# Optimization experiments

Hardware: AMD Instinct MI355X
Metric: run time of the kernel (lower is better)

Reference implementation:

```python
import jax, jax.numpy as jnp
import numpy as np

KERNEL = 10   # kernel_size (asserted == 10 in the original)
HEADS = 4
BN_SCALE = 1.0 / np.sqrt(1.0 + 1e-5)  # eval-mode BatchNorm1d (running mean 0, var 1, affine 1/0)


def get_dct_matrix(N):
    k = np.arange(N)[:, None].astype(np.float64)
    i = np.arange(N)[None, :].astype(np.float64)
    w = np.full((N, 1), np.sqrt(2.0 / N))
    w[0, 0] = np.sqrt(1.0 / N)
    dct_m = w * np.cos(np.pi * (i + 0.5) * k / N)
    idct_m = np.linalg.inv(dct_m)
    return dct_m.astype(np.float32), idct_m.astype(np.float32)


def conv1d(x, w):  # x [B,C,L], w [O,I,K], valid, no bias
    return jax.lax.conv_general_dilated(x, w, (1,), 'VALID',
                                        dimension_numbers=('NCH', 'OIH', 'NCH'))


def conv_stack(x, w1, w2):  # Conv1d(k=6) -> ReLU -> Conv1d(k=5) -> ReLU
    return jax.nn.relu(conv1d(jax.nn.relu(conv1d(x, w1)), w2))


# vmap over the 4 heads' weights -> [H,B,D,L]
heads_conv = jax.vmap(conv_stack, in_axes=(None, 0, 0))


def _forward(src, cq1, cq2, ck1, ck2, lw, lb, giw, gia, gib, gbw, gba, gbb,
             gow, goa, gob, dct_n, output_n, input_n):
    bs, in_feat = src.shape[0], src.shape[2]
    src = src[:, :input_n]                                   # [B,50,48]
    src_key = jnp.swapaxes(src, 1, 2)[:, :, :input_n - output_n]  # [B,48,25]
    src_query = jnp.swapaxes(src, 1, 2)[:, :, -KERNEL:]           # [B,48,10]

    dct_np, idct_np = get_dct_matrix(KERNEL + output_n)
    dct_m = jnp.asarray(dct_np)
    idct_m = jnp.asarray(idct_np)

    vn = input_n - KERNEL - output_n + 1  # 16 overlapping value windows
    vl = KERNEL + output_n                # window length 35
    idx = np.arange(vl)[None, :] + np.arange(vn)[:, None]    # [16,35]
    windows = src[:, idx]                                    # [B,16,35,48]
    # DCT per window then flatten per-joint coeffs: [B,16,48*dct_n]
    val = jnp.einsum('dv,bnvf->bndf', dct_m[:dct_n], windows)
    src_value = jnp.swapaxes(val, 2, 3).reshape(bs, vn, -1)  # [B,16,480]

    key_h = heads_conv(src_key / 1000.0, ck1, ck2)           # [H,B,512,16]
    query_h = heads_conv(src_query / 1000.0, cq1, cq2)       # [H,B,512,1]

    # sum-normalized (non-softmax) attention
    score = jnp.einsum('hbdq,hbdk->hbqk', query_h, key_h) + 1e-15  # [H,B,1,16]
    att_w = score / jnp.sum(score, axis=3, keepdims=True)
    dct_att = jnp.einsum('hbk,bkf->hbf', att_w[:, :, 0], src_value)  # [H,B,480]
    dct_att = dct_att.reshape(HEADS, bs, in_feat, dct_n)
    att_cat = jnp.transpose(dct_att, (1, 0, 2, 3)).reshape(bs, HEADS * in_feat, dct_n)
    # Linear over the concatenated head/joint axis: [B,48,dct_n]
    att_lin = jnp.einsum('bmd,nm->bnd', att_cat, lw) + lb[None, :, None]

    # last kernel_size frames + last frame repeated output_n times
    gather_idx = np.concatenate([np.arange(input_n - KERNEL, input_n),
                                 np.full(output_n, input_n - 1)])
    input_gcn = src[:, gather_idx]                           # [B,35,48]
    dct_in = jnp.einsum('dv,bvf->bfd', dct_m[:dct_n], input_gcn)  # [B,48,10]
    dct_in = jnp.concatenate([dct_in, att_lin], axis=-1)     # [B,48,20]

    # GCN (Mao et al. style): learnable adjacency [48,48], eval-mode BN, tanh
    def gc(h, a, w, b):
        return jnp.einsum('nm,bmf->bnf', a, h @ w) + b

    y = jnp.tanh(gc(dct_in, gia, giw, gib) * BN_SCALE)       # [B,48,512]
    for s in range(gbw.shape[0]):
        r = y
        for j in range(2):
            y = jnp.tanh(gc(y, gba[s, j], gbw[s, j], gbb[s, j]) * BN_SCALE)
        y = y + r
    dct_out = gc(y, goa, gow, gob) + dct_in                  # [B,48,20]

    out_gcn = jnp.einsum('vd,bnd->bvn', idct_m[:, :dct_n], dct_out[:, :, :dct_n])  # [B,35,48]
    return out_gcn[:, :, None, :]                            # [B,35,itera=1,48]


def setup_inputs() -> dict:
    key = jax.random.key(0)
    ks = jax.random.split(key, 16)
    bs, in_feat, d_model, dct_n = 256, 48, 512, 10
    s = 0.05
    return {
        'src': jax.random.normal(ks[0], (bs, 50, in_feat), jnp.float32) * 1000.0,
        'convQ_w1': jax.random.normal(ks[1], (HEADS, d_model, in_feat, 6), jnp.float32) * s,
        'convQ_w2': jax.random.normal(ks[2], (HEADS, d_model, d_model, 5), jnp.float32) * s,
        'convK_w1': jax.random.normal(ks[3], (HEADS, d_model, in_feat, 6), jnp.float32) * s,
        'convK_w2': jax.random.normal(ks[4], (HEADS, d_model, d_model, 5), jnp.float32) * s,
        'linear_w': jax.random.normal(ks[5], (in_feat, HEADS * in_feat), jnp.float32) * s,
        'linear_b': jax.random.normal(ks[6], (in_feat,), jnp.float32) * s,
        'gc_in_w': jax.random.normal(ks[7], (2 * dct_n, d_model), jnp.float32) * s,
        'gc_in_att': jax.random.normal(ks[8], (in_feat, in_feat), jnp.float32) * s,
        'gc_in_b': jax.random.normal(ks[9], (d_model,), jnp.float32) * s,
        'gcb_w': jax.random.normal(ks[10], (2, 2, d_model, d_model), jnp.float32) * s,
        'gcb_att': jax.random.normal(ks[11], (2, 2, in_feat, in_feat), jnp.float32) * s,
        'gcb_b': jax.random.normal(ks[12], (2, 2, d_model), jnp.float32) * s,
        'gc_out_w': jax.random.normal(ks[13], (d_model, 2 * dct_n), jnp.float32) * s,
        'gc_out_att': jax.random.normal(ks[14], (in_feat, in_feat), jnp.float32) * s,
        'gc_out_b': jax.random.normal(ks[15], (2 * dct_n,), jnp.float32) * s,
        'dct_n': 10, 'output_n': 25, 'input_n': 50, 'itera': 1,
    }


def reference(src, convQ_w1, convQ_w2, convK_w1, convK_w2, linear_w, linear_b,
              gc_in_w, gc_in_att, gc_in_b, gcb_w, gcb_att, gcb_b,
              gc_out_w, gc_out_att, gc_out_b, dct_n, output_n, input_n, itera):
    # itera=1 path only (itera>1 in the original references undefined attrs)
    return _forward(src, convQ_w1, convQ_w2, convK_w1, convK_w2, linear_w, linear_b,
                    gc_in_w, gc_in_att, gc_in_b, gcb_w, gcb_att, gcb_b,
                    gc_out_w, gc_out_att, gc_out_b, dct_n, output_n, input_n)
```

## Files before the change

### kernel.cpp

```cpp
#include <hip/hip_runtime.h>
#include <math.h>

static constexpr float BN_SCALE_F = 0.9999950000374997f;

typedef __bf16 bf16;
typedef bf16 bf16x8 __attribute__((ext_vector_type(8)));
typedef bf16 bf16x4 __attribute__((ext_vector_type(4)));
typedef float floatx4 __attribute__((ext_vector_type(4)));

#define GLOBAL_AS __attribute__((address_space(1)))
#define LDS_AS __attribute__((address_space(3)))

__device__ __forceinline__ float tanh_fast(float x) {
    const float e = __expf(2.f * x);
    return 1.f - 2.f / (e + 1.f);
}

__global__ __launch_bounds__(256) void k_prep(
    const float* __restrict__ src, const float* __restrict__ cq1,
    const float* __restrict__ ck1, const float* __restrict__ cq2,
    const float* __restrict__ ck2, const float* __restrict__ gbw,
    const float* __restrict__ giw, const float* __restrict__ gow,
    const float* __restrict__ gba, float* __restrict__ dct10,
    bf16* __restrict__ srcbf, bf16* __restrict__ w1tq, bf16* __restrict__ w1tk,
    bf16* __restrict__ w2tq, bf16* __restrict__ w2tk, bf16* __restrict__ gbwF,
    bf16* __restrict__ giwF, bf16* __restrict__ gowT, bf16* __restrict__ gbaP) {
    __shared__ __align__(16) float lds[10240];
    int bb = blockIdx.x;
    const int t = threadIdx.x;
    if (bb < 2) {
        int id = bb * 256 + t;
        if (id < 350) {
            int k = id / 35, i = id % 35;
            double w = (k == 0) ? sqrt(1.0 / 35.0) : sqrt(2.0 / 35.0);
            dct10[id] = (float)(w * cos(3.14159265358979323846 * (i + 0.5) * k / 35.0));
        }
        return;
    }
    bb -= 2;
    if (bb < 601) {
        const int id4 = (bb * 256 + t) * 4;
        if (id4 + 3 < 614400) {
            const float4 v = *(const float4*)(src + id4);
            bf16x4 ov;
            ov[0] = (bf16)v.x; ov[1] = (bf16)v.y;
            ov[2] = (bf16)v.z; ov[3] = (bf16)v.w;
            *(bf16x4*)(srcbf + id4) = ov;
        } else if (id4 < 614656) {
#pragma unroll
            for (int j = 0; j < 4; ++j) {
                const int id = id4 + j;
                if (id < 614656) srcbf[id] = (bf16)(id < 614400 ? src[id] : 0.f);
            }
        }
        return;
    }
    bb -= 601;
    if (bb < 1280) {
        const bool isQ = bb < 640;
        const float* w = isQ ? cq1 : ck1;
        bf16* wt = isQ ? w1tq : w1tk;
        const int lb = isQ ? bb : bb - 640;
        const int id4 = (lb * 256 + t) * 4;
        const int ho = id4 / 320, c0 = id4 % 320;
        bf16x4 ov;
#pragma unroll
        for (int j = 0; j < 4; ++j) {
            const int c = c0 + j;
            const float v =
                (c < 288) ? w[(long)ho * 288 + (c % 48) * 6 + (c / 48)] * 1e-3f : 0.f;
            ov[j] = (bf16)v;
        }
        *(bf16x4*)(wt + id4) = ov;
        return;
    }
    bb -= 1280;
    if (bb < 1024) {
        const bool isQ = bb < 512;
        const int rb = isQ ? bb : bb - 512;
        const float* wrow = (isQ ? cq2 : ck2) + (long)rb * 4 * 2560;
        bf16* orow = (isQ ? w2tq : w2tk) + (long)rb * 4 * 2560;
        float4* l4 = (float4*)lds;
        const float4* w4 = (const float4*)wrow;
#pragma unroll
        for (int i = 0; i < 10; ++i) l4[t + i * 256] = w4[t + i * 256];
        __syncthreads();
        for (int c = t * 4; c < 10240; c += 1024) {
            const int r = c / 2560, cc = c % 2560;
            const int k = cc >> 9, ii = cc & 511;
            bf16x4 ov;
#pragma unroll
            for (int j = 0; j < 4; ++j)
                ov[j] = (bf16)lds[r * 2560 + (ii + j) * 5 + k];
            *(bf16x4*)(orow + c) = ov;
        }
        return;
    }
    bb -= 1024;
    if (bb < 256) {
        const int l = bb >> 6, tile = bb & 63;
        const int tr = tile >> 3, tc = tile & 7;
        const float* in = gbw + (long)l * 262144;
        bf16* o = gbwF + (long)l * 262144;
#pragma unroll
        for (int r = 0; r < 16; ++r) {
            const int kl = (t >> 6) * 16 + r, ml = t & 63;
            lds[kl * 65 + ml] = in[(long)(tr * 64 + kl) * 512 + tc * 64 + ml];
        }
        __syncthreads();
        for (int j = t; j < 4096; j += 256) {
            const int q = j >> 9, r4 = j & 511;
            const int gl = q >> 2, sl = (q >> 1) & 1, jt = q & 1;
            const int lane = r4 >> 3, e = r4 & 7;
            const int fr = lane & 15, fq = lane >> 4;
            const int kk = sl * 32 + fq * 8 + e;
            const int ff = gl * 32 + jt * 16 + fr;
            o[(long)(tc * 2 + gl) * 16384 + (long)(tr * 2 + sl) * 1024 + jt * 512 + r4] =
                (bf16)lds[kk * 65 + ff];
        }
        return;
    }
    bb -= 256;
    if (bb < 32) {
        const int id4 = (bb * 256 + t) * 4;
        const int g = id4 >> 11, r2 = id4 & 2047;
        const int s = r2 >> 10, r3 = r2 & 1023;
        const int jt = r3 >> 9, r4 = r3 & 511;
        const int lane = r4 >> 3, e0 = r4 & 7;
        const int fr = lane & 15, fq = lane >> 4;
        const int f = g * 32 + jt * 16 + fr;
        bf16x4 ov;
#pragma unroll
        for (int j = 0; j < 4; ++j) {
            const int k = s * 32 + fq * 8 + e0 + j;
            ov[j] = (bf16)(k < 20 ? giw[k * 512 + f] : 0.f);
        }
        *(bf16x4*)(giwF + id4) = ov;
        return;
    }
    bb -= 32;
    if (bb < 16) {
        const int id4 = (bb * 256 + t) * 4;
        const int d = id4 >> 9, k0 = id4 & 511;
        bf16x4 ov;
#pragma unroll
        for (int j = 0; j < 4; ++j)
            ov[j] = (bf16)(d < 20 ? gow[(k0 + j) * 20 + d] : 0.f);
        *(bf16x4*)(gowT + id4) = ov;
        return;
    }
    bb -= 16;
    {
        const int id4 = (bb * 256 + t) * 4;
        const int l = id4 / 3072, r = id4 % 3072;
        const int n = r >> 6, m0 = r & 63;
        bf16x4 ov;
#pragma unroll
        for (int j = 0; j < 4; ++j) {
            const int m = m0 + j;
            ov[j] = (bf16)(m < 48 ? gba[l * 2304 + n * 48 + m] : 0.f);
        }
        *(bf16x4*)(gbaP + id4) = ov;
    }
}

__global__ __launch_bounds__(256) void k_conv1(
    const bf16* __restrict__ w1tk, const bf16* __restrict__ w1tq,
    const bf16* __restrict__ srcbf, bf16* __restrict__ r1k,
    bf16* __restrict__ r1q) {
    int bx, by, bz;
    const bf16* A;
    bf16* C;
    int NT, toff;
    long cStr;
    {
        const int i = blockIdx.x;
        if (i < 1280) {
            bz = i / 320;
            const int r = i % 320;
            bx = r % 40;
            by = r / 40;
            A = w1tk; C = r1k; NT = 20; toff = 0; cStr = 2621440L;
        } else {
            const int j = i - 1280;
            bz = j / 80;
            const int r = j % 80;
            bx = r % 10;
            by = r / 10;
            A = w1tq; C = r1q; NT = 5; toff = 40; cStr = 655360L;
        }
    }
    __shared__ bf16 As[64 * 64];
    __shared__ bf16 Bs[128 * 64];
    const int tid = threadIdx.x;
    const int wave = tid >> 6;
    const int lane = tid & 63;
    const int wm = (wave & 1) * 32;
    const int wn = (wave >> 1) * 64;
    const int m0 = by * 64;
    const int n0 = bx * 128;
    A += (long)bz * (512L * 320);

    const int srow = lane >> 3;
    const int gch = (lane & 7) ^ srow;
    const bf16* aptr[2];
    const bf16* bptr[4];
#pragma unroll
    for (int i = 0; i < 2; ++i) {
        const int ar = wave * 16 + i * 8 + srow;
        aptr[i] = A + (long)(m0 + ar) * 320 + gch * 8;
    }
#pragma unroll
    for (int i = 0; i < 4; ++i) {
        const int ar = wave * 32 + i * 8 + srow;
        const int n = n0 + ar;
        const long bbase = (long)(n / NT) * 2400 + (long)((n % NT) + toff) * 48;
        bptr[i] = srcbf + bbase + gch * 8;
    }

    floatx4 acc[4][2];
#pragma unroll
    for (int j = 0; j < 4; ++j)
#pragma unroll
        for (int i = 0; i < 2; ++i) acc[j][i] = (floatx4){0.f, 0.f, 0.f, 0.f};

    const int fr = lane & 15;
    const int fq = lane >> 4;
    const int fx = lane & 7;

    for (int k0 = 0; k0 < 320; k0 += 64) {
#pragma unroll
        for (int i = 0; i < 2; ++i)
            __builtin_amdgcn_global_load_lds(
                (const GLOBAL_AS void*)(aptr[i] + k0),
                (LDS_AS void*)(As + (wave * 16 + i * 8) * 64), 16, 0, 0);
#pragma unroll
        for (int i = 0; i < 4; ++i)
            __builtin_amdgcn_global_load_lds(
                (const GLOBAL_AS void*)(bptr[i] + k0),
                (LDS_AS void*)(Bs + (wave * 32 + i * 8) * 64), 16, 0, 0);
        __syncthreads();
#pragma unroll
        for (int kk = 0; kk < 2; ++kk) {
            bf16x8 af[2], bfr[4];
#pragma unroll
            for (int im = 0; im < 2; ++im)
                af[im] = *(const bf16x8*)(As + (wm + im * 16 + fr) * 64 +
                                          ((((kk << 2) + fq) ^ fx) << 3));
#pragma unroll
            for (int in = 0; in < 4; ++in)
                bfr[in] = *(const bf16x8*)(Bs + (wn + in * 16 + fr) * 64 +
                                           ((((kk << 2) + fq) ^ fx) << 3));
#pragma unroll
            for (int in = 0; in < 4; ++in)
#pragma unroll
                for (int im = 0; im < 2; ++im)
                    acc[in][im] = __builtin_amdgcn_mfma_f32_16x16x32_bf16(
                        af[im], bfr[in], acc[in][im], 0, 0, 0);
        }
        __syncthreads();
    }
#pragma unroll
    for (int in = 0; in < 4; ++in) {
        const long n = n0 + wn + in * 16 + fr;
#pragma unroll
        for (int im = 0; im < 2; ++im) {
            floatx4 v = acc[in][im];
            const long m = m0 + wm + im * 16 + (fq << 2);
            v.x = fmaxf(v.x, 0.f);
            v.y = fmaxf(v.y, 0.f);
            v.z = fmaxf(v.z, 0.f);
            v.w = fmaxf(v.w, 0.f);
            bf16* Cp = C + (long)bz * cStr + n * 512 + m;
            bf16x4 ov;
            ov[0] = (bf16)v.x;
            ov[1] = (bf16)v.y;
            ov[2] = (bf16)v.z;
            ov[3] = (bf16)v.w;
            *(bf16x4*)Cp = ov;
        }
    }
}

__global__ __launch_bounds__(256) void k_conv2(
    const bf16* __restrict__ w2tk, const bf16* __restrict__ r1k,
    bf16* __restrict__ keyh, const bf16* __restrict__ w2tq,
    const bf16* __restrict__ r1q, bf16* __restrict__ qh) {
    const int K = 2560;
    int bx, by, bz;
    const bf16 *A, *B;
    bf16* C;
    bool kMode;
    long aStr, bStr, cStr;
    {
        const int i = blockIdx.x;
        if (i < 1024) {
            const int slot = i & 7;
            bz = slot >> 1;
            const int half = slot & 1;
            const int j = i >> 3;
            bx = half * 16 + (j & 15);
            by = j >> 4;
            A = w2tk; B = r1k; C = keyh; kMode = true;
            aStr = 512L * 2560; bStr = 2621440L; cStr = 2097152L;
        } else {
            const int j = i - 1024;
            bz = j >> 4;
            const int r = j & 15;
            bx = r & 1;
            by = r >> 1;
            A = w2tq; B = r1q; C = qh; kMode = false;
            aStr = 512L * 2560; bStr = 655360L; cStr = 131072L;
        }
    }
    __shared__ bf16 As[64 * 64];
    __shared__ bf16 Bs[160 * 64];
    const int tid = threadIdx.x;
    const int wave = tid >> 6;
    const int lane = tid & 63;
    const int wm = (wave & 1) * 32;
    const int wn = (wave >> 1) * 64;
    const int m0 = by * 64;
    const int n0 = bx * 128;
    A += (long)bz * aStr;
    B += (long)bz * bStr;

    const int srow = lane >> 3;
    const int gch = (lane & 7) ^ srow;
    const bf16* aptr[2];
#pragma unroll
    for (int i = 0; i < 2; ++i) {
        const int ar = wave * 16 + i * 8 + srow;
        aptr[i] = A + (long)(m0 + ar) * K + gch * 8;
    }

    floatx4 acc[4][2];
#pragma unroll
    for (int j = 0; j < 4; ++j)
#pragma unroll
        for (int i = 0; i < 2; ++i) acc[j][i] = (floatx4){0.f, 0.f, 0.f, 0.f};

    const int fr = lane & 15;
    const int fq = lane >> 4;
    const int fx = lane & 7;

    if (kMode) {
        const bf16* bptrK[5];
        int ldsBK[5];
#pragma unroll
        for (int j = 0; j < 5; ++j) {
            const int rloc = wave * 40 + j * 8 + srow;
            const int brel = rloc / 20, pos = rloc % 20;
            bptrK[j] = B + ((long)((bx * 8 + brel) * 20 + pos)) * 512 +
                       ((lane & 7) ^ (pos & 7)) * 8;
            ldsBK[j] = rloc * 64 + (lane & 7) * 8;
        }
        const int bq = wn >> 4;
        for (int c0i = 0; c0i < 8; ++c0i) {
            const int c0 = c0i * 64;
#pragma unroll
            for (int w = 0; w < 5; ++w) {
                const int k0 = w * 512 + c0;
#pragma unroll
                for (int i = 0; i < 2; ++i)
                    __builtin_amdgcn_global_load_lds(
                        (const GLOBAL_AS void*)(aptr[i] + k0),
                        (LDS_AS void*)(As + (wave * 16 + i * 8) * 64), 16, 0, 0);
                if (w == 0) {
#pragma unroll
                    for (int j = 0; j < 5; ++j)
                        __builtin_amdgcn_global_load_lds(
                            (const GLOBAL_AS void*)(bptrK[j] + c0),
                            (LDS_AS void*)(Bs + ldsBK[j]), 16, 0, 0);
                }
                __syncthreads();
#pragma unroll
                for (int kk = 0; kk < 2; ++kk) {
                    bf16x8 af[2], bfr[4];
#pragma unroll
                    for (int im = 0; im < 2; ++im)
                        af[im] = *(const bf16x8*)(As + (wm + im * 16 + fr) * 64 +
                                                  ((((kk << 2) + fq) ^ fx) << 3));
#pragma unroll
                    for (int nt = 0; nt < 4; ++nt) {
                        const int row = (bq + nt) * 20 + fr + w;
                        bfr[nt] = *(const bf16x8*)(
                            Bs + row * 64 +
                            ((((kk << 2) + fq) ^ ((fr + w) & 7)) << 3));
                    }
#pragma unroll
                    for (int nt = 0; nt < 4; ++nt)
#pragma unroll
                        for (int im = 0; im < 2; ++im)
                            acc[nt][im] = __builtin_amdgcn_mfma_f32_16x16x32_bf16(
                                af[im], bfr[nt], acc[nt][im], 0, 0, 0);
                }
                __syncthreads();
            }
        }
    } else {
        const bf16* bptr[4];
#pragma unroll
        for (int i = 0; i < 4; ++i) {
            const int ar = wave * 32 + i * 8 + srow;
            bptr[i] = B + (long)(n0 + ar) * K + gch * 8;
        }
        for (int k0 = 0; k0 < K; k0 += 64) {
#pragma unroll
            for (int i = 0; i < 2; ++i)
                __builtin_amdgcn_global_load_lds(
                    (const GLOBAL_AS void*)(aptr[i] + k0),
                    (LDS_AS void*)(As + (wave * 16 + i * 8) * 64), 16, 0, 0);
#pragma unroll
            for (int i = 0; i < 4; ++i)
                __builtin_amdgcn_global_load_lds(
                    (const GLOBAL_AS void*)(bptr[i] + k0),
                    (LDS_AS void*)(Bs + (wave * 32 + i * 8) * 64), 16, 0, 0);
            __syncthreads();
#pragma unroll
            for (int kk = 0; kk < 2; ++kk) {
                bf16x8 af[2], bfr[4];
#pragma unroll
                for (int im = 0; im < 2; ++im)
                    af[im] = *(const bf16x8*)(As + (wm + im * 16 + fr) * 64 +
                                              ((((kk << 2) + fq) ^ fx) << 3));
#pragma unroll
                for (int in = 0; in < 4; ++in)
                    bfr[in] = *(const bf16x8*)(Bs + (wn + in * 16 + fr) * 64 +
                                               ((((kk << 2) + fq) ^ fx) << 3));
#pragma unroll
                for (int in = 0; in < 4; ++in)
#pragma unroll
                    for (int im = 0; im < 2; ++im)
                        acc[in][im] = __builtin_amdgcn_mfma_f32_16x16x32_bf16(
                            af[im], bfr[in], acc[in][im], 0, 0, 0);
            }
            __syncthreads();
        }
    }
#pragma unroll
    for (int in = 0; in < 4; ++in) {
        const long n = n0 + wn + in * 16 + fr;
#pragma unroll
        for (int im = 0; im < 2; ++im) {
            floatx4 v = acc[in][im];
            const long m = m0 + wm + im * 16 + (fq << 2);
            v.x = fmaxf(v.x, 0.f);
            v.y = fmaxf(v.y, 0.f);
            v.z = fmaxf(v.z, 0.f);
            v.w = fmaxf(v.w, 0.f);
            bf16* Cp = C + (long)bz * cStr + n * 512 + m;
            bf16x4 ov;
            ov[0] = (bf16)v.x;
            ov[1] = (bf16)v.y;
            ov[2] = (bf16)v.z;
            ov[3] = (bf16)v.w;
            *(bf16x4*)Cp = ov;
        }
    }
}

__global__ __launch_bounds__(512) void k_att(
    const bf16* __restrict__ qh, const bf16* __restrict__ keyh,
    const float* __restrict__ src, const float* __restrict__ dct10,
    const float* __restrict__ lw, const float* __restrict__ lb,
    const float* __restrict__ gia, float* __restrict__ dctin,
    bf16* __restrict__ z0) {
    const int b = blockIdx.x;
    const int t = threadIdx.x;
    __shared__ float BIG[9216];
    __shared__ float WD[2400];
    __shared__ float D[350];
    __shared__ float L[1920];
    __shared__ float dinS[960];
    __shared__ float sS[64];
    __shared__ float awS[64];

    {
        const int g = t >> 3, lane = t & 7;
        const int h = g >> 4, tt = g & 15;
        const bf16* q = qh + ((long)h * 256 + b) * 512 + lane * 64;
        const bf16* kr = keyh + (long)h * 2097152 + ((long)b * 16 + tt) * 512 + lane * 64;
        float p = 0.f;
#pragma unroll
        for (int i = 0; i < 8; ++i) {
            const bf16x8 qv = *(const bf16x8*)(q + i * 8);
            const bf16x8 kv = *(const bf16x8*)(kr + i * 8);
#pragma unroll
            for (int j = 0; j < 8; ++j) p = fmaf((float)qv[j], (float)kv[j], p);
        }
        p += __shfl_down(p, 4, 8);
        p += __shfl_down(p, 2, 8);
        p += __shfl_down(p, 1, 8);
        if (lane == 0) sS[g] = p + 1e-15f;
    }
    for (int i = t; i < 2400; i += 512) WD[i] = src[(long)b * 2400 + i];
    for (int i = t; i < 350; i += 512) D[i] = dct10[i];
    __syncthreads();
    if (t < 4) {
        float s = 0.f;
#pragma unroll
        for (int k = 0; k < 16; ++k) s += sS[t * 16 + k];
        const float inv = 1.f / s;
#pragma unroll
        for (int k = 0; k < 16; ++k) awS[t * 16 + k] = sS[t * 16 + k] * inv;
    }
    __syncthreads();
    if (t < 480) {
        const int f = t / 10, d = t % 10;
        float dreg[35];
#pragma unroll
        for (int v = 0; v < 35; ++v) dreg[v] = D[d * 35 + v];
#pragma unroll 2
        for (int n = 0; n < 16; ++n) {
            float acc = 0.f;
#pragma unroll
            for (int v = 0; v < 35; ++v)
                acc = fmaf(dreg[v], WD[(n + v) * 48 + f], acc);
            BIG[n * 480 + t] = acc;
        }
        float acc = 0.f;
#pragma unroll
        for (int v = 0; v < 10; ++v)
            acc = fmaf(dreg[v], WD[(40 + v) * 48 + f], acc);
        float cs = 0.f;
#pragma unroll
        for (int v = 10; v < 35; ++v) cs += dreg[v];
        acc = fmaf(cs, WD[49 * 48 + f], acc);
        dinS[f * 20 + d] = acc;
        dctin[(long)b * 960 + f * 20 + d] = acc;
    }
    __syncthreads();
    for (int p = 0; p < 4; ++p) {
        const int idx = t + p * 512;
        if (idx < 1920) {
            const int h = idx / 480, j = idx % 480;
            float acc = 0.f;
#pragma unroll
            for (int k = 0; k < 16; ++k)
                acc = fmaf(awS[h * 16 + k], BIG[k * 480 + j], acc);
            L[idx] = acc;
        }
    }
    __syncthreads();
    for (int i = t; i < 9216; i += 512) BIG[i] = lw[i];
    for (int i = t; i < 2304; i += 512) WD[i] = gia[i];
    __syncthreads();
    if (t < 480) {
        const int n = t / 10, d = t % 10;
        float acc = lb[n];
#pragma unroll
        for (int h = 0; h < 4; ++h)
#pragma unroll
            for (int f = 0; f < 48; ++f)
                acc = fmaf(BIG[n * 192 + h * 48 + f], L[h * 480 + f * 10 + d], acc);
        dinS[n * 20 + 10 + d] = acc;
        dctin[(long)b * 960 + n * 20 + 10 + d] = acc;
    }
    __syncthreads();
    for (int p = 0; p < 2; ++p) {
        const int idx = t + p * 512;
        if (idx < 960) {
            const int n = idx / 20, d = idx % 20;
            float acc = 0.f;
#pragma unroll
            for (int m = 0; m < 48; ++m)
                acc = fmaf(WD[n * 48 + m], dinS[m * 20 + d], acc);
            z0[((long)b * 48 + n) * 64 + d] = (bf16)acc;
        }
    }
    for (int i = t; i < 2112; i += 512) {
        const int n = i / 44, c = 20 + i % 44;
        z0[((long)b * 48 + n) * 64 + c] = (bf16)0.f;
    }
}

template <bool TOUT, int S>
__device__ __forceinline__ void gcn_matmul3(
    const bf16* __restrict__ zSrc, const bf16* __restrict__ Wf,
    const float* __restrict__ bias, const bf16* __restrict__ resT,
    bf16* __restrict__ outS, const int wave, const int lane) {
    const int fr = lane & 15, fq = lane >> 4;
    const int f0 = wave * 32;
    floatx4 acc[3][2];
#pragma unroll
    for (int it = 0; it < 3; ++it)
#pragma unroll
        for (int jt = 0; jt < 2; ++jt) acc[it][jt] = (floatx4){0.f, 0.f, 0.f, 0.f};
    const bf16* wp = Wf + (long)wave * (S * 1024) + (lane << 3);
    bf16x8 w0[4], w1[4];
    constexpr int PRE = (S < 3) ? S : 3;
#pragma unroll
    for (int s = 0; s < PRE; ++s) {
        w0[s] = *(const bf16x8*)(wp + s * 1024);
        w1[s] = *(const bf16x8*)(wp + s * 1024 + 512);
    }
#pragma unroll
    for (int s = 0; s < S; ++s) {
        bf16x8 af[3];
#pragma unroll
        for (int it = 0; it < 3; ++it)
            af[it] = *(const bf16x8*)(zSrc + (it * 16 + fr) * 520 + s * 32 + fq * 8);
        if (s + 3 < S) {
            const int ns = (s + 3) & 3;
            w0[ns] = *(const bf16x8*)(wp + (s + 3) * 1024);
            w1[ns] = *(const bf16x8*)(wp + (s + 3) * 1024 + 512);
        }
        const int sl = s & 3;
#pragma unroll
        for (int it = 0; it < 3; ++it) {
            acc[it][0] = __builtin_amdgcn_mfma_f32_16x16x32_bf16(af[it], w0[sl],
                                                                acc[it][0], 0, 0, 0);
            acc[it][1] = __builtin_amdgcn_mfma_f32_16x16x32_bf16(af[it], w1[sl],
                                                                acc[it][1], 0, 0, 0);
        }
    }
#pragma unroll
    for (int jt = 0; jt < 2; ++jt) {
        const int f = f0 + jt * 16 + fr;
        const float bv = bias[f];
#pragma unroll
        for (int it = 0; it < 3; ++it) {
            const int ir0 = it * 16 + fq * 4;
            float v[4];
#pragma unroll
            for (int r = 0; r < 4; ++r)
                v[r] = tanh_fast((acc[it][jt][r] + bv) * BN_SCALE_F);
            if (resT) {
                const bf16x4 rv = *(const bf16x4*)(resT + f * 48 + ir0);
#pragma unroll
                for (int r = 0; r < 4; ++r) v[r] += (float)rv[r];
            }
            if (TOUT) {
                bf16x4 ov;
#pragma unroll
                for (int r = 0; r < 4; ++r) ov[r] = (bf16)v[r];
                *(bf16x4*)(outS + f * 48 + ir0) = ov;
            } else {
#pragma unroll
                for (int r = 0; r < 4; ++r)
                    outS[(ir0 + r) * 520 + f] = (bf16)v[r];
            }
        }
    }
}

__device__ __forceinline__ void gcn_attmul2(const bf16* __restrict__ gA,
                                            const bf16* __restrict__ YinT,
                                            bf16* __restrict__ zOut,
                                            const int wave, const int lane) {
    const int fr = lane & 15, fq = lane >> 4;
    const int f0 = wave * 32;
    floatx4 acc[3][2];
#pragma unroll
    for (int it = 0; it < 3; ++it)
#pragma unroll
        for (int jt = 0; jt < 2; ++jt) acc[it][jt] = (floatx4){0.f, 0.f, 0.f, 0.f};
    bf16x8 af0[3], af1[3], bv0[2], bv1[2];
#pragma unroll
    for (int it = 0; it < 3; ++it) {
        af0[it] = *(const bf16x8*)(gA + (it * 16 + fr) * 64 + fq * 8);
        af1[it] = *(const bf16x8*)(gA + (it * 16 + fr) * 64 + 32 + fq * 8);
    }
#pragma unroll
    for (int jt = 0; jt < 2; ++jt) {
        const int f = f0 + jt * 16 + fr;
        bv0[jt] = *(const bf16x8*)(YinT + f * 48 + fq * 8);
        bv1[jt] = *(const bf16x8*)(YinT + f * 48 + 32 + fq * 8);
    }
#pragma unroll
    for (int it = 0; it < 3; ++it)
#pragma unroll
        for (int jt = 0; jt < 2; ++jt) {
            acc[it][jt] = __builtin_amdgcn_mfma_f32_16x16x32_bf16(af0[it], bv0[jt],
                                                                 acc[it][jt], 0, 0, 0);
            acc[it][jt] = __builtin_amdgcn_mfma_f32_16x16x32_bf16(af1[it], bv1[jt],
                                                                 acc[it][jt], 0, 0, 0);
        }
#pragma unroll
    for (int jt = 0; jt < 2; ++jt) {
        const int f = f0 + jt * 16 + fr;
#pragma unroll
        for (int it = 0; it < 3; ++it)
#pragma unroll
            for (int r = 0; r < 4; ++r)
                zOut[(it * 16 + fq * 4 + r) * 520 + f] = (bf16)acc[it][jt][r];
    }
}

__global__ __launch_bounds__(1024) void k_gcn(
    const bf16* __restrict__ z0, const bf16* __restrict__ giwF,
    const float* __restrict__ gib, const bf16* __restrict__ gbwF,
    const bf16* __restrict__ gbaP, const float* __restrict__ gbb,
    const float* __restrict__ goa, const bf16* __restrict__ gowT,
    const float* __restrict__ gob, const float* __restrict__ dctin,
    const float* __restrict__ dct10, float* __restrict__ out) {
    const int b = blockIdx.x;
    const int t = threadIdx.x;
    const int wave = t >> 6, lane = t & 63;
    __shared__ __align__(16) bf16 yaS[24976];
    __shared__ __align__(16) bf16 ybS[24592];
    __shared__ __align__(16) bf16 zS[48 * 520];

    if (t < 384) {
        const int r = t >> 3, c = t & 7;
        *(bf16x8*)(zS + r * 520 + c * 8) =
            *(const bf16x8*)(z0 + ((long)b * 48 + r) * 64 + c * 8);
    } else if (t < 400) {
        yaS[24576 + (t - 384)] = (bf16)0.f;
    } else if (t < 416) {
        ybS[24576 + (t - 400)] = (bf16)0.f;
    }
    __syncthreads();
    gcn_matmul3<true, 2>(zS, giwF, gib, nullptr, yaS, wave, lane);
    __syncthreads();

#pragma unroll
    for (int l = 0; l < 4; ++l) {
        const bf16* YinT = (l == 0 || l == 3) ? yaS : ybS;
        gcn_attmul2(gbaP + l * 3072, YinT, zS, wave, lane);
        __syncthreads();
        const bf16* Res = (l == 1) ? yaS : (l == 3 ? ybS : nullptr);
        if (l < 3)
            gcn_matmul3<true, 16>(zS, gbwF + (long)l * 262144, gbb + l * 512,
                                  Res, (l < 2) ? ybS : yaS, wave, lane);
        else
            gcn_matmul3<false, 16>(zS, gbwF + 3L * 262144, gbb + 3 * 512, Res,
                                   yaS, wave, lane);
        __syncthreads();
    }
    float* T2 = (float*)ybS;
    float* dS = ((float*)ybS) + 960;
    float* goaS = ((float*)ybS) + 1920;
    float* Df = ((float*)ybS) + 4224;
    if (t < 384) {
        const int fr2 = lane & 15, fq2 = lane >> 4;
        const int it = wave >> 1, jt = wave & 1;
        floatx4 accT = (floatx4){0.f, 0.f, 0.f, 0.f};
        const bf16* ap = yaS + (it * 16 + fr2) * 520 + fq2 * 8;
        const bf16* gp = gowT + (long)(jt * 16 + fr2) * 512 + fq2 * 8;
        for (int k0 = 0; k0 < 512; k0 += 32) {
            const bf16x8 av = *(const bf16x8*)(ap + k0);
            const bf16x8 gv = *(const bf16x8*)(gp + k0);
            accT = __builtin_amdgcn_mfma_f32_16x16x32_bf16(av, gv, accT, 0, 0, 0);
        }
        const int d = jt * 16 + fr2;
        if (d < 20) {
#pragma unroll
            for (int r = 0; r < 4; ++r) {
                const int m = it * 16 + fq2 * 4 + r;
                T2[m * 20 + d] = accT[r];
            }
        }
    } else {
        for (int i = t - 384; i < 2304; i += 640) goaS[i] = goa[i];
        for (int i = t - 384; i < 350; i += 640) Df[i] = dct10[i];
    }
    __syncthreads();
    if (t < 960) {
        const int n = t / 20, d = t % 20;
        float acc = gob[d] + dctin[(long)b * 960 + t];
#pragma unroll
        for (int m = 0; m < 48; ++m)
            acc = fmaf(goaS[n * 48 + m], T2[m * 20 + d], acc);
        dS[t] = acc;
    }
    __syncthreads();
    for (int e = t; e < 1680; e += 1024) {
        const int v = e / 48, n = e % 48;
        float acc = 0.f;
#pragma unroll
        for (int d = 0; d < 10; ++d)
            acc = fmaf(Df[d * 35 + v], dS[n * 20 + d], acc);
        out[(long)b * 1680 + e] = acc;
    }
}

static constexpr size_t WS_DCT10 = 0;
static constexpr size_t WS_ATTW = 1536;
static constexpr size_t WS_QH = WS_ATTW + 65536;
static constexpr size_t WS_DCTIN = WS_QH + 2097152;
static constexpr size_t WS_DCTOUT = WS_DCTIN + 983040;
static constexpr size_t WS_SRCVAL = WS_DCTOUT + 983040;
static constexpr size_t WS_PAD0 = WS_SRCVAL + 7864320;
static constexpr size_t WS_GOWT = WS_PAD0;
static constexpr size_t WS_GBAP = WS_PAD0 + 32768;
static constexpr size_t WS_SRCBF = WS_PAD0 + 8388608;
static constexpr size_t WS_W1TQ = WS_SRCBF + 1229824;
static constexpr size_t WS_W1TK = WS_W1TQ + 1310720;
static constexpr size_t WS_W2TQ = WS_W1TK + 1310720;
static constexpr size_t WS_W2TK = WS_W2TQ + 10485760;
static constexpr size_t WS_GBWT = WS_W2TK + 10485760;
static constexpr size_t WS_R1K = WS_GBWT + 2097152;
static constexpr size_t WS_R1Q = WS_R1K + 20971520;
static constexpr size_t WS_T = WS_R1Q + 5242880;
static constexpr size_t WS_GIWP = WS_T + 50331648;
static constexpr size_t WS_KEYH = WS_T;
static constexpr size_t WS_Z0 = WS_T + 17825792;

extern "C" void kernel_launch(void* const* d_in, const int* in_sizes, int n_in,
                              void* d_out, int out_size, void* d_ws,
                              size_t ws_size, hipStream_t stream) {
    const float* src = (const float*)d_in[0];
    const float* cq1 = (const float*)d_in[1];
    const float* cq2 = (const float*)d_in[2];
    const float* ck1 = (const float*)d_in[3];
    const float* ck2 = (const float*)d_in[4];
    const float* lw = (const float*)d_in[5];
    const float* lb = (const float*)d_in[6];
    const float* giw = (const float*)d_in[7];
    const float* gia = (const float*)d_in[8];
    const float* gib = (const float*)d_in[9];
    const float* gbw = (const float*)d_in[10];
    const float* gba = (const float*)d_in[11];
    const float* gbb = (const float*)d_in[12];
    const float* gow = (const float*)d_in[13];
    const float* goa = (const float*)d_in[14];
    const float* gob = (const float*)d_in[15];
    float* out = (float*)d_out;
    char* ws = (char*)d_ws;

    float* dct10 = (float*)(ws + WS_DCT10);
    bf16* qh = (bf16*)(ws + WS_QH);
    float* dctin = (float*)(ws + WS_DCTIN);
    bf16* keyh = (bf16*)(ws + WS_KEYH);
    bf16* srcbf = (bf16*)(ws + WS_SRCBF);
    bf16* w1tq = (bf16*)(ws + WS_W1TQ);
    bf16* w1tk = (bf16*)(ws + WS_W1TK);
    bf16* w2tq = (bf16*)(ws + WS_W2TQ);
    bf16* w2tk = (bf16*)(ws + WS_W2TK);
    bf16* gbwF = (bf16*)(ws + WS_GBWT);
    bf16* r1k = (bf16*)(ws + WS_R1K);
    bf16* r1q = (bf16*)(ws + WS_R1Q);
    bf16* giwF = (bf16*)(ws + WS_GIWP);
    bf16* gowT = (bf16*)(ws + WS_GOWT);
    bf16* gbaP = (bf16*)(ws + WS_GBAP);
    bf16* z0 = (bf16*)(ws + WS_Z0);

    k_prep<<<3223, 256, 0, stream>>>(src, cq1, ck1, cq2, ck2, gbw, giw, gow,
                                     gba, dct10, srcbf, w1tq, w1tk, w2tq,
                                     w2tk, gbwF, giwF, gowT, gbaP);

    k_conv1<<<1600, 256, 0, stream>>>(w1tk, w1tq, srcbf, r1k, r1q);

    k_conv2<<<1088, 256, 0, stream>>>(w2tk, r1k, keyh, w2tq, r1q, qh);

    k_att<<<256, 512, 0, stream>>>(qh, keyh, src, dct10, lw, lb, gia, dctin, z0);

    k_gcn<<<256, 1024, 0, stream>>>(z0, giwF, gib, gbwF, gbaP, gbb, goa, gowT,
                                    gob, dctin, dct10, out);
}
```

Before: 292.7 us.

## Move weight-repack work from prep kernel into conv1 launch to overlap with GEMM

The conv2, GCN and graph-attention weight repacking blocks move out of the prep kernel and into extra blocks of the conv1 GEMM launch. They can then run concurrently with the conv1 tiles instead of serialising before them. The repack blocks are also shrunk in LDS footprint (fewer rows per block, gbw tile processed in halves) so the fused kernel keeps a 24KB shared buffer and better occupancy. The attention kernel preloads lw and gia into dedicated LDS arrays at the start, removing one barrier-separated reload phase at the cost of more shared memory per block.

After: 305.3 us. 4.3% more time.

```diff
diff --git a/kernel.cpp b/kernel.cpp
--- a/kernel.cpp
+++ b/kernel.cpp
@@ -18,14 +18,8 @@
 
 __global__ __launch_bounds__(256) void k_prep(
     const float* __restrict__ src, const float* __restrict__ cq1,
-    const float* __restrict__ ck1, const float* __restrict__ cq2,
-    const float* __restrict__ ck2, const float* __restrict__ gbw,
-    const float* __restrict__ giw, const float* __restrict__ gow,
-    const float* __restrict__ gba, float* __restrict__ dct10,
-    bf16* __restrict__ srcbf, bf16* __restrict__ w1tq, bf16* __restrict__ w1tk,
-    bf16* __restrict__ w2tq, bf16* __restrict__ w2tk, bf16* __restrict__ gbwF,
-    bf16* __restrict__ giwF, bf16* __restrict__ gowT, bf16* __restrict__ gbaP) {
-    __shared__ __align__(16) float lds[10240];
+    const float* __restrict__ ck1, float* __restrict__ dct10,
+    bf16* __restrict__ srcbf, bf16* __restrict__ w1tq, bf16* __restrict__ w1tk) {
     int bb = blockIdx.x;
     const int t = threadIdx.x;
     if (bb < 2) {
@@ -56,7 +50,7 @@
         return;
     }
     bb -= 601;
-    if (bb < 1280) {
+    {
         const bool isQ = bb < 640;
         const float* w = isQ ? cq1 : ck1;
         bf16* wt = isQ ? w1tq : w1tk;
@@ -72,129 +66,143 @@
             ov[j] = (bf16)v;
         }
         *(bf16x4*)(wt + id4) = ov;
-        return;
-    }
-    bb -= 1280;
-    if (bb < 1024) {
-        const bool isQ = bb < 512;
-        const int rb = isQ ? bb : bb - 512;
-        const float* wrow = (isQ ? cq2 : ck2) + (long)rb * 4 * 2560;
-        bf16* orow = (isQ ? w2tq : w2tk) + (long)rb * 4 * 2560;
-        float4* l4 = (float4*)lds;
-        const float4* w4 = (const float4*)wrow;
-#pragma unroll
-        for (int i = 0; i < 10; ++i) l4[t + i * 256] = w4[t + i * 256];
-        __syncthreads();
-        for (int c = t * 4; c < 10240; c += 1024) {
-            const int r = c / 2560, cc = c % 2560;
-            const int k = cc >> 9, ii = cc & 511;
-            bf16x4 ov;
-#pragma unroll
-            for (int j = 0; j < 4; ++j)
-                ov[j] = (bf16)lds[r * 2560 + (ii + j) * 5 + k];
-            *(bf16x4*)(orow + c) = ov;
-        }
-        return;
-    }
-    bb -= 1024;
-    if (bb < 256) {
-        const int l = bb >> 6, tile = bb & 63;
-        const int tr = tile >> 3, tc = tile & 7;
-        const float* in = gbw + (long)l * 262144;
-        bf16* o = gbwF + (long)l * 262144;
-#pragma unroll
-        for (int r = 0; r < 16; ++r) {
-            const int kl = (t >> 6) * 16 + r, ml = t & 63;
-            lds[kl * 65 + ml] = in[(long)(tr * 64 + kl) * 512 + tc * 64 + ml];
-        }
-        __syncthreads();
-        for (int j = t; j < 4096; j += 256) {
-            const int q = j >> 9, r4 = j & 511;
-            const int gl = q >> 2, sl = (q >> 1) & 1, jt = q & 1;
-            const int lane = r4 >> 3, e = r4 & 7;
-            const int fr = lane & 15, fq = lane >> 4;
-            const int kk = sl * 32 + fq * 8 + e;
-            const int ff = gl * 32 + jt * 16 + fr;
-            o[(long)(tc * 2 + gl) * 16384 + (long)(tr * 2 + sl) * 1024 + jt * 512 + r4] =
-                (bf16)lds[kk * 65 + ff];
-        }
-        return;
-    }
-    bb -= 256;
-    if (bb < 32) {
-        const int id4 = (bb * 256 + t) * 4;
-        const int g = id4 >> 11, r2 = id4 & 2047;
-        const int s = r2 >> 10, r3 = r2 & 1023;
-        const int jt = r3 >> 9, r4 = r3 & 511;
-        const int lane = r4 >> 3, e0 = r4 & 7;
-        const int fr = lane & 15, fq = lane >> 4;
-        const int f = g * 32 + jt * 16 + fr;
-        bf16x4 ov;
-#pragma unroll
-        for (int j = 0; j < 4; ++j) {
-            const int k = s * 32 + fq * 8 + e0 + j;
-            ov[j] = (bf16)(k < 20 ? giw[k * 512 + f] : 0.f);
-        }
-        *(bf16x4*)(giwF + id4) = ov;
-        return;
-    }
-    bb -= 32;
-    if (bb < 16) {
-        const int id4 = (bb * 256 + t) * 4;
-        const int d = id4 >> 9, k0 = id4 & 511;
-        bf16x4 ov;
-#pragma unroll
-        for (int j = 0; j < 4; ++j)
-            ov[j] = (bf16)(d < 20 ? gow[(k0 + j) * 20 + d] : 0.f);
-        *(bf16x4*)(gowT + id4) = ov;
-        return;
-    }
-    bb -= 16;
-    {
-        const int id4 = (bb * 256 + t) * 4;
-        const int l = id4 / 3072, r = id4 % 3072;
-        const int n = r >> 6, m0 = r & 63;
-        bf16x4 ov;
-#pragma unroll
-        for (int j = 0; j < 4; ++j) {
-            const int m = m0 + j;
-            ov[j] = (bf16)(m < 48 ? gba[l * 2304 + n * 48 + m] : 0.f);
-        }
-        *(bf16x4*)(gbaP + id4) = ov;
     }
 }
 
-__global__ __launch_bounds__(256) void k_conv1(
+__global__ __launch_bounds__(256) void k_conv1p(
     const bf16* __restrict__ w1tk, const bf16* __restrict__ w1tq,
     const bf16* __restrict__ srcbf, bf16* __restrict__ r1k,
-    bf16* __restrict__ r1q) {
+    bf16* __restrict__ r1q, const float* __restrict__ cq2,
+    const float* __restrict__ ck2, const float* __restrict__ gbw,
+    const float* __restrict__ giw, const float* __restrict__ gow,
+    const float* __restrict__ gba, bf16* __restrict__ w2tq,
+    bf16* __restrict__ w2tk, bf16* __restrict__ gbwF,
+    bf16* __restrict__ giwF, bf16* __restrict__ gowT,
+    bf16* __restrict__ gbaP) {
+    __shared__ __align__(16) char smem[24576];
+    const int t = threadIdx.x;
+    int i = blockIdx.x;
+    if (i >= 1600) {
+        i -= 1600;
+        float* lds = (float*)smem;
+        if (i < 2048) {
+            const bool isQ = i < 1024;
+            const int lb = isQ ? i : i - 1024;
+            const float* wrow = (isQ ? cq2 : ck2) + (long)lb * 2 * 2560;
+            bf16* orow = (isQ ? w2tq : w2tk) + (long)lb * 2 * 2560;
+            float4* l4 = (float4*)lds;
+            const float4* w4 = (const float4*)wrow;
+#pragma unroll
+            for (int j = 0; j < 5; ++j) l4[t + j * 256] = w4[t + j * 256];
+            __syncthreads();
+            for (int c = t * 4; c < 5120; c += 1024) {
+                const int r = c / 2560, cc = c % 2560;
+                const int k = cc >> 9, ii = cc & 511;
+                bf16x4 ov;
+#pragma unroll
+                for (int j = 0; j < 4; ++j)
+                    ov[j] = (bf16)lds[r * 2560 + (ii + j) * 5 + k];
+                *(bf16x4*)(orow + c) = ov;
+            }
+            return;
+        }
+        i -= 2048;
+        if (i < 256) {
+            const int l = i >> 6, tile = i & 63;
+            const int tr = tile >> 3, tc = tile & 7;
+            const float* in = gbw + (long)l * 262144;
+            bf16* o = gbwF + (long)l * 262144;
+#pragma unroll
+            for (int half = 0; half < 2; ++half) {
+#pragma unroll
+                for (int r = 0; r < 8; ++r) {
+                    const int kl = (t >> 6) * 8 + r, ml = t & 63;
+                    lds[kl * 65 + ml] =
+                        in[(long)(tr * 64 + half * 32 + kl) * 512 + tc * 64 + ml];
+                }
+                __syncthreads();
+                for (int j = t; j < 2048; j += 256) {
+                    const int q = j >> 9, r4 = j & 511;
+                    const int gl = q >> 1, jt = q & 1;
+                    const int lane = r4 >> 3, e = r4 & 7;
+                    const int fr = lane & 15, fq = lane >> 4;
+                    const int kk = fq * 8 + e;
+                    const int ff = gl * 32 + jt * 16 + fr;
+                    o[(long)(tc * 2 + gl) * 16384 +
+                      (long)(tr * 2 + half) * 1024 + jt * 512 + r4] =
+                        (bf16)lds[kk * 65 + ff];
+                }
+                __syncthreads();
+            }
+            return;
+        }
+        i -= 256;
+        if (i < 32) {
+            const int id4 = (i * 256 + t) * 4;
+            const int g = id4 >> 11, r2 = id4 & 2047;
+            const int s = r2 >> 10, r3 = r2 & 1023;
+            const int jt = r3 >> 9, r4 = r3 & 511;
+            const int lane = r4 >> 3, e0 = r4 & 7;
+            const int fr = lane & 15, fq = lane >> 4;
+            const int f = g * 32 + jt * 16 + fr;
+            bf16x4 ov;
+#pragma unroll
+            for (int j = 0; j < 4; ++j) {
+                const int k = s * 32 + fq * 8 + e0 + j;
+                ov[j] = (bf16)(k < 20 ? giw[k * 512 + f] : 0.f);
+            }
+            *(bf16x4*)(giwF + id4) = ov;
+            return;
+        }
+        i -= 32;
+        if (i < 16) {
+            const int id4 = (i * 256 + t) * 4;
+            const int d = id4 >> 9, k0 = id4 & 511;
+            bf16x4 ov;
+#pragma unroll
+            for (int j = 0; j < 4; ++j)
+                ov[j] = (bf16)(d < 20 ? gow[(k0 + j) * 20 + d] : 0.f);
+            *(bf16x4*)(gowT + id4) = ov;
+            return;
+        }
+        i -= 16;
+        {
+            const int id4 = (i * 256 + t) * 4;
+            const int l = id4 / 3072, r = id4 % 3072;
+            const int n = r >> 6, m0 = r & 63;
+            bf16x4 ov;
+#pragma unroll
+            for (int j = 0; j < 4; ++j) {
+                const int m = m0 + j;
+                ov[j] = (bf16)(m < 48 ? gba[l * 2304 + n * 48 + m] : 0.f);
+            }
+            *(bf16x4*)(gbaP + id4) = ov;
+        }
+        return;
+    }
+    bf16* As = (bf16*)smem;
+    bf16* Bs = (bf16*)(smem + 8192);
     int bx, by, bz;
     const bf16* A;
     bf16* C;
     int NT, toff;
     long cStr;
-    {
-        const int i = blockIdx.x;
-        if (i < 1280) {
-            bz = i / 320;
-            const int r = i % 320;
-            bx = r % 40;
-            by = r / 40;
-            A = w1tk; C = r1k; NT = 20; toff = 0; cStr = 2621440L;
-        } else {
-            const int j = i - 1280;
-            bz = j / 80;
-            const int r = j % 80;
-            bx = r % 10;
-            by = r / 10;
-            A = w1tq; C = r1q; NT = 5; toff = 40; cStr = 655360L;
-        }
-    }
-    __shared__ bf16 As[64 * 64];
-    __shared__ bf16 Bs[128 * 64];
-    const int tid = threadIdx.x;
-    const int wave = tid >> 6;
-    const int lane = tid & 63;
+    if (i < 1280) {
+        bz = i / 320;
+        const int r = i % 320;
+        bx = r % 40;
+        by = r / 40;
+        A = w1tk; C = r1k; NT = 20; toff = 0; cStr = 2621440L;
+    } else {
+        const int j = i - 1280;
+        bz = j / 80;
+        const int r = j % 80;
+        bx = r % 10;
+        by = r / 10;
+        A = w1tq; C = r1q; NT = 5; toff = 40; cStr = 655360L;
+    }
+    const int wave = t >> 6;
+    const int lane = t & 63;
     const int wm = (wave & 1) * 32;
     const int wn = (wave >> 1) * 64;
     const int m0 = by * 64;
@@ -206,23 +214,23 @@
     const bf16* aptr[2];
     const bf16* bptr[4];
 #pragma unroll
-    for (int i = 0; i < 2; ++i) {
-        const int ar = wave * 16 + i * 8 + srow;
-        aptr[i] = A + (long)(m0 + ar) * 320 + gch * 8;
-    }
-#pragma unroll
-    for (int i = 0; i < 4; ++i) {
-        const int ar = wave * 32 + i * 8 + srow;
+    for (int j = 0; j < 2; ++j) {
+        const int ar = wave * 16 + j * 8 + srow;
+        aptr[j] = A + (long)(m0 + ar) * 320 + gch * 8;
+    }
+#pragma unroll
+    for (int j = 0; j < 4; ++j) {
+        const int ar = wave * 32 + j * 8 + srow;
         const int n = n0 + ar;
         const long bbase = (long)(n / NT) * 2400 + (long)((n % NT) + toff) * 48;
-        bptr[i] = srcbf + bbase + gch * 8;
+        bptr[j] = srcbf + bbase + gch * 8;
     }
 
     floatx4 acc[4][2];
 #pragma unroll
     for (int j = 0; j < 4; ++j)
 #pragma unroll
-        for (int i = 0; i < 2; ++i) acc[j][i] = (floatx4){0.f, 0.f, 0.f, 0.f};
+        for (int q = 0; q < 2; ++q) acc[j][q] = (floatx4){0.f, 0.f, 0.f, 0.f};
 
     const int fr = lane & 15;
     const int fq = lane >> 4;
@@ -230,15 +238,15 @@
 
     for (int k0 = 0; k0 < 320; k0 += 64) {
 #pragma unroll
-        for (int i = 0; i < 2; ++i)
+        for (int j = 0; j < 2; ++j)
             __builtin_amdgcn_global_load_lds(
-                (const GLOBAL_AS void*)(aptr[i] + k0),
-                (LDS_AS void*)(As + (wave * 16 + i * 8) * 64), 16, 0, 0);
-#pragma unroll
-        for (int i = 0; i < 4; ++i)
+                (const GLOBAL_AS void*)(aptr[j] + k0),
+                (LDS_AS void*)(As + (wave * 16 + j * 8) * 64), 16, 0, 0);
+#pragma unroll
+        for (int j = 0; j < 4; ++j)
             __builtin_amdgcn_global_load_lds(
-                (const GLOBAL_AS void*)(bptr[i] + k0),
-                (LDS_AS void*)(Bs + (wave * 32 + i * 8) * 64), 16, 0, 0);
+                (const GLOBAL_AS void*)(bptr[j] + k0),
+                (LDS_AS void*)(Bs + (wave * 32 + j * 8) * 64), 16, 0, 0);
         __syncthreads();
 #pragma unroll
         for (int kk = 0; kk < 2; ++kk) {
@@ -469,6 +477,8 @@
     const int b = blockIdx.x;
     const int t = threadIdx.x;
     __shared__ float BIG[9216];
+    __shared__ float lwS[9216];
+    __shared__ float giaS[2304];
     __shared__ float WD[2400];
     __shared__ float D[350];
     __shared__ float L[1920];
@@ -496,6 +506,8 @@
     }
     for (int i = t; i < 2400; i += 512) WD[i] = src[(long)b * 2400 + i];
     for (int i = t; i < 350; i += 512) D[i] = dct10[i];
+    for (int i = t; i < 9216; i += 512) lwS[i] = lw[i];
+    for (int i = t; i < 2304; i += 512) giaS[i] = gia[i];
     __syncthreads();
     if (t < 4) {
         float s = 0.f;
@@ -543,9 +555,6 @@
         }
     }
     __syncthreads();
-    for (int i = t; i < 9216; i += 512) BIG[i] = lw[i];
-    for (int i = t; i < 2304; i += 512) WD[i] = gia[i];
-    __syncthreads();
     if (t < 480) {
         const int n = t / 10, d = t % 10;
         float acc = lb[n];
@@ -553,7 +562,7 @@
         for (int h = 0; h < 4; ++h)
 #pragma unroll
             for (int f = 0; f < 48; ++f)
-                acc = fmaf(BIG[n * 192 + h * 48 + f], L[h * 480 + f * 10 + d], acc);
+                acc = fmaf(lwS[n * 192 + h * 48 + f], L[h * 480 + f * 10 + d], acc);
         dinS[n * 20 + 10 + d] = acc;
         dctin[(long)b * 960 + n * 20 + 10 + d] = acc;
     }
@@ -565,7 +574,7 @@
             float acc = 0.f;
 #pragma unroll
             for (int m = 0; m < 48; ++m)
-                acc = fmaf(WD[n * 48 + m], dinS[m * 20 + d], acc);
+                acc = fmaf(giaS[n * 48 + m], dinS[m * 20 + d], acc);
             z0[((long)b * 48 + n) * 64 + d] = (bf16)acc;
         }
     }
@@ -837,11 +846,11 @@
     bf16* gbaP = (bf16*)(ws + WS_GBAP);
     bf16* z0 = (bf16*)(ws + WS_Z0);
 
-    k_prep<<<3223, 256, 0, stream>>>(src, cq1, ck1, cq2, ck2, gbw, giw, gow,
-                                     gba, dct10, srcbf, w1tq, w1tk, w2tq,
-                                     w2tk, gbwF, giwF, gowT, gbaP);
-
-    k_conv1<<<1600, 256, 0, stream>>>(w1tk, w1tq, srcbf, r1k, r1q);
+    k_prep<<<1883, 256, 0, stream>>>(src, cq1, ck1, dct10, srcbf, w1tq, w1tk);
+
+    k_conv1p<<<3964, 256, 0, stream>>>(w1tk, w1tq, srcbf, r1k, r1q, cq2, ck2,
+                                       gbw, giw, gow, gba, w2tq, w2tk, gbwF,
+                                       giwF, gowT, gbaP);
 
     k_conv2<<<1088, 256, 0, stream>>>(w2tk, r1k, keyh, w2tq, r1q, qh);
 
```
